# Optimization experiments

Hardware: AMD Instinct MI355X
Metric: run time of the kernel (lower is better)

The kernel has to match this reference:

```python
import jax, jax.numpy as jnp
import numpy as np

N = 32768      # tokens
E = 2048       # embedding_dim
V = 256        # vq_dim
K = 256        # codebook size (levels=[256] -> single level, log2 K = 8)
HID = 1024     # condition MLP hidden dim
LOG2K = 8      # log2_num_embeddings
N_MID = 4      # condition_layer - 2 middle blocks
BN_EPS = 1e-5


def _normalize(x):
    return x / (jnp.linalg.norm(x, axis=-1, keepdims=True) + 1e-6)


def _bn(x, g, b):
    # BatchNorm1d, training-mode batch statistics over the codebook rows
    m = x.mean(0)
    v = x.var(0)
    return g * (x - m) * jax.lax.rsqrt(v + BN_EPS) + b


def _codebook(w0, b0, g0, be0, wm, bm, gm, bem, wL, bL):
    # get_bvectors(8, 256): binary expansion of 0..255, width 8 (no pad needed)
    ints = jnp.arange(K)
    bits = ((ints[:, None] >> jnp.arange(LOG2K - 1, -1, -1)[None, :]) & 1).astype(jnp.float32)
    x = jax.nn.relu(_bn(bits @ w0 + b0, g0, be0))
    for i in range(N_MID):
        x = jax.nn.relu(_bn(x @ wm[i] + bm[i], gm[i], bem[i]))
    return x @ wL + bL  # [K, V]


def setup_inputs() -> dict:
    key = jax.random.key(0)
    ks = jax.random.split(key, 8)
    def lin(k, fan_in, shape):
        return (jax.random.normal(k, shape, jnp.float32) / np.sqrt(fan_in)).astype(jnp.float32)
    return {
        "h_in": jax.random.normal(ks[0], (N, E), jnp.float32),
        "temp": jnp.array([0.3], jnp.float32),
        "proj_w": lin(ks[1], E, (E, V)), "proj_b": jnp.zeros((V,), jnp.float32),
        "pinv_w": lin(ks[2], V, (V, E)), "pinv_b": jnp.zeros((E,), jnp.float32),
        "w0": lin(ks[3], LOG2K, (LOG2K, HID)), "b0": jnp.zeros((HID,), jnp.float32),
        "g0": jnp.ones((HID,), jnp.float32), "be0": jnp.zeros((HID,), jnp.float32),
        "wm": lin(ks[4], HID, (N_MID, HID, HID)), "bm": jnp.zeros((N_MID, HID), jnp.float32),
        "gm": jnp.ones((N_MID, HID), jnp.float32), "bem": jnp.zeros((N_MID, HID), jnp.float32),
        "wL": lin(ks[5], HID, (HID, V)), "bL": jnp.zeros((V,), jnp.float32),
    }


def reference(h_in, temp, proj_w, proj_b, pinv_w, pinv_b,
              w0, b0, g0, be0, wm, bm, gm, bem, wL, bL):
    # forward(h_in, mode='eval', temperature=1, level=256); levels=[256] -> idx_all=1
    h = _normalize(h_in @ proj_w + proj_b)                          # proj + sphere normalize, [N, V]
    embed = _normalize(_codebook(w0, b0, g0, be0, wm, bm, gm, bem, wL, bL))  # [K, V]

    # attention(): distance logits with temperature-scaled detached term
    sim = h @ embed.T                                               # [N, K]
    alpha = 1.0 / temp ** 2
    distances = -2.0 * (alpha - 1.0) * jax.lax.stop_gradient(sim) - 2.0 * sim
    A = jax.nn.softmax(-distances, axis=1)                          # [N, K]

    k_code, k_p = jax.random.split(jax.random.key(42))
    code = jax.random.categorical(k_code, -distances, axis=-1)      # multinomial(A, 1), [N]
    onehot = jax.nn.one_hot(code, K, dtype=A.dtype)
    c = onehot * (1.0 - A) + (1.0 - onehot) * (-A)
    A2 = A + jax.lax.stop_gradient(c)                               # fwd value == onehot
    h_vq = h + A2 @ embed - jax.lax.stop_gradient(h)                # straight-through quantize
    vq_loss = jnp.linalg.norm(h_vq - h, axis=-1).mean()             # idx_all == 1

    # select = (0 < p) & (p < 1) since idx=0, idx_all=1
    p = jax.random.uniform(k_p, (h.shape[0],))
    select = (0.0 < p) & (p < 1.0)
    quantized = h_vq * select[:, None].astype(h_vq.dtype)
    probs = A * select[:, None].astype(A.dtype)
    vq_code = code * select.astype(code.dtype)

    quantized_inv = quantized @ pinv_w + pinv_b                     # [N, E]
    return quantized_inv, vq_code, quantized, probs, vq_loss
```

## Files before the change

### kernel.cpp

```cpp
#include <hip/hip_runtime.h>
#include <hip/hip_bf16.h>
#include <stdint.h>
#include <stddef.h>

#ifndef PARTITIONABLE
#define PARTITIONABLE 1
#endif

typedef __attribute__((ext_vector_type(8))) short short8;
typedef __attribute__((ext_vector_type(4))) short short4v;
typedef __attribute__((ext_vector_type(4))) float f32x4;

__host__ __device__ __forceinline__ uint32_t rotl32(uint32_t x, int d){ return (x<<d)|(x>>(32-d)); }

__host__ __device__ __forceinline__ void tf4(uint32_t&x0, uint32_t&x1, int r0,int r1,int r2,int r3){
  x0+=x1; x1=rotl32(x1,r0); x1^=x0;
  x0+=x1; x1=rotl32(x1,r1); x1^=x0;
  x0+=x1; x1=rotl32(x1,r2); x1^=x0;
  x0+=x1; x1=rotl32(x1,r3); x1^=x0;
}
__host__ __device__ __forceinline__ void threefry2x32(uint32_t k0,uint32_t k1,uint32_t x0,uint32_t x1,
                                                      uint32_t&y0,uint32_t&y1){
  uint32_t ks2 = k0^k1^0x1BD11BDAu;
  x0+=k0; x1+=k1;
  tf4(x0,x1,13,15,26,6);  x0+=k1;  x1+=ks2+1u;
  tf4(x0,x1,17,29,16,24); x0+=ks2; x1+=k0+2u;
  tf4(x0,x1,13,15,26,6);  x0+=k0;  x1+=k1+3u;
  tf4(x0,x1,17,29,16,24); x0+=k1;  x1+=ks2+4u;
  tf4(x0,x1,13,15,26,6);  x0+=ks2; x1+=k0+5u;
  y0=x0; y1=x1;
}

__device__ __forceinline__ uint32_t random_bits32(uint32_t k0,uint32_t k1,uint32_t idx, uint32_t half){
#if PARTITIONABLE
  uint32_t y0,y1; threefry2x32(k0,k1, 0u, idx, y0,y1);
  (void)half;
  return y0 ^ y1;
#else
  uint32_t y0,y1;
  if (idx < half) { threefry2x32(k0,k1, idx, idx+half, y0,y1); return y0; }
  else            { threefry2x32(k0,k1, idx-half, idx, y0,y1); return y1; }
#endif
}

__device__ __forceinline__ unsigned short bf16_rne(float x){
  unsigned u = __float_as_uint(x);
  unsigned r = (u + 0x7FFFu + ((u>>16)&1u)) >> 16;
  return (unsigned short)r;
}
__device__ __forceinline__ float bf16_tof(unsigned short h){
  return __uint_as_float(((unsigned)h)<<16);
}
__device__ __forceinline__ void split8(const float* src, short8& hi, short8& lo){
  #pragma unroll
  for (int e=0;e<8;e++){
    unsigned short h = bf16_rne(src[e]);
    hi[e] = (short)h;
    lo[e] = (short)bf16_rne(src[e] - bf16_tof(h));
  }
}
__device__ __forceinline__ void split4(const float* src, short4v& hi, short4v& lo){
  #pragma unroll
  for (int e=0;e<4;e++){
    unsigned short h = bf16_rne(src[e]);
    hi[e] = (short)h;
    lo[e] = (short)bf16_rne(src[e] - bf16_tof(h));
  }
}

__device__ __forceinline__ void gll16(const void* g, void* l){
  __builtin_amdgcn_global_load_lds(
      (const __attribute__((address_space(1))) unsigned int*)g,
      (__attribute__((address_space(3))) unsigned int*)l, 16, 0, 0);
}

__device__ __forceinline__ void mk1_gemm(const float* __restrict__ A, int lda,
                                         const unsigned short* __restrict__ packB,
                                         int K, char* smem, f32x4 (&acc)[2][4]){
  const int tid=threadIdx.x, lane=tid&63, wv=tid>>6;
  const int wr=wv>>2, wc=wv&3;
  const int arow=tid>>3, aseg=tid&7, swA=(arow>>1)&3;
  unsigned short* Ahi=(unsigned short*)smem;
  unsigned short* Alo=(unsigned short*)(smem+4096);
  unsigned short* Bhi=(unsigned short*)(smem+8192);
  unsigned short* Blo=(unsigned short*)(smem+24576);
  const int NT=K/32;
  const int sA = arow*32 + ((aseg>>1)^swA)*8 + (aseg&1)*4;
  const int seg = wv*2;

  float4 av = *(const float4*)(A + (size_t)arow*lda + aseg*4);
  for(int t=0;t<NT;t++){
    __syncthreads();
    {
      float af[4]={av.x,av.y,av.z,av.w}; short4v vh,vl; split4(af,vh,vl);
      *(short4v*)&Ahi[sA]=vh; *(short4v*)&Alo[sA]=vl;
      const unsigned short* src = packB + (size_t)t*16384;
      #pragma unroll
      for(int q=0;q<2;q++){
        gll16(src + (seg+q)*512 + lane*8,        (char*)Bhi + (seg+q)*1024);
        gll16(src + 8192 + (seg+q)*512 + lane*8, (char*)Blo + (seg+q)*1024);
      }
      if (t+1<NT) av = *(const float4*)(A + (size_t)arow*lda + (t+1)*32 + aseg*4);
    }
    __syncthreads();
    short8 ah[2],al[2],bh[4],bl[4];
    const int kg=lane>>4;
    #pragma unroll
    for(int i=0;i<2;i++){
      const int r = wr*32 + i*16 + (lane&15);
      const int offA = r*32 + ((kg ^ ((r>>1)&3))*8);
      ah[i]=*(const short8*)&Ahi[offA]; al[i]=*(const short8*)&Alo[offA];
    }
    #pragma unroll
    for(int j=0;j<4;j++){
      const int c = wc*64 + j*16 + (lane&15);
      const int offB = c*32 + ((kg ^ ((c>>1)&3))*8);
      bh[j]=*(const short8*)&Bhi[offB]; bl[j]=*(const short8*)&Blo[offB];
    }
    #pragma unroll
    for(int i=0;i<2;i++)
      #pragma unroll
      for(int j=0;j<4;j++){
        acc[i][j]=__builtin_amdgcn_mfma_f32_16x16x32_bf16(ah[i],bh[j],acc[i][j],0,0,0);
        acc[i][j]=__builtin_amdgcn_mfma_f32_16x16x32_bf16(ah[i],bl[j],acc[i][j],0,0,0);
        acc[i][j]=__builtin_amdgcn_mfma_f32_16x16x32_bf16(al[i],bh[j],acc[i][j],0,0,0);
      }
  }
}

__device__ __forceinline__ void bn_block_t(float (&acc)[4], int col0,
                                           const float* __restrict__ gma,
                                           const float* __restrict__ bta,
                                           float* __restrict__ Yt,
                                           float* Zs, float* red, float* mcol, float* vcol){
  const int r = threadIdx.x;
  #pragma unroll
  for (int j=0;j<4;j++) Zs[r*5+j] = acc[j];
  __syncthreads();
  if (r < 16){
    const int rl = r & 3, j = r >> 2;
    float s = 0.f;
    for (int rr=rl; rr<256; rr+=4) s += Zs[rr*5+j];
    red[rl*4+j] = s;
  }
  __syncthreads();
  if (r < 4)
    mcol[r] = (red[0*4+r]+red[1*4+r]+red[2*4+r]+red[3*4+r]) * (1.0f/256.0f);
  __syncthreads();
  if (r < 16){
    const int rl = r & 3, j = r >> 2;
    const float m = mcol[j];
    float s2 = 0.f;
    for (int rr=rl; rr<256; rr+=4){ float d = Zs[rr*5+j]-m; s2 += d*d; }
    red[rl*4+j] = s2;
  }
  __syncthreads();
  if (r < 4)
    vcol[r] = (red[0*4+r]+red[1*4+r]+red[2*4+r]+red[3*4+r]) * (1.0f/256.0f);
  __syncthreads();
  #pragma unroll
  for (int j=0;j<4;j++){
    const int c = col0 + j;
    const float scale = gma[c] * rsqrtf(vcol[j] + 1e-5f);
    const float sh = bta[c];
    const float v = (acc[j]-mcol[j])*scale + sh;
    Yt[(size_t)c*256 + r] = v > 0.f ? v : 0.f;
  }
}

__global__ __launch_bounds__(256) void prep_kernel(
    const float* __restrict__ proj_w, unsigned short* __restrict__ packW,
    const float* __restrict__ w0, const float* __restrict__ b0,
    const float* __restrict__ g0, const float* __restrict__ be0,
    float* __restrict__ XtA){
  __shared__ float Zs[256*5];
  __shared__ float red[16], mcol[4], vcol[4];
  const int b = blockIdx.x, tid = threadIdx.x;
  {
    const int t = b>>2, s = b&3, c = tid;
    const int g = s ^ ((c>>1)&3);
    const float* p = proj_w + (size_t)(t*32 + g*8)*256 + c;
    float bf[8];
    #pragma unroll
    for(int e=0;e<8;e++) bf[e]=p[(size_t)e*256];
    short8 h,l; split8(bf,h,l);
    unsigned short* dst = packW + (size_t)t*16384 + c*32 + s*8;
    *(short8*)dst = h;
    *(short8*)(dst+8192) = l;
  }
  {
    const int col0 = b*4;
    float acc[4];
    #pragma unroll
    for (int j=0;j<4;j++) acc[j] = b0[col0+j];
    #pragma unroll
    for (int jj=0;jj<8;jj++){
      if ((tid >> (7-jj)) & 1){
        #pragma unroll
        for (int j=0;j<4;j++) acc[j] += w0[jj*1024 + col0 + j];
      }
    }
    bn_block_t(acc, col0, g0, be0, XtA, Zs, red, mcol, vcol);
  }
}

__global__ __launch_bounds__(256) void mlp_layer2_kernel(
    const float* __restrict__ Xt, const float* __restrict__ W,
    const float* __restrict__ bias,
    const float* __restrict__ gma, const float* __restrict__ bta,
    float* __restrict__ Yt){
  __shared__ float Ws[1024*2];
  __shared__ float Zs[256*3];
  __shared__ float red[8], mcol[2], vcol[2];
  const int r = threadIdx.x;
  const int col0 = blockIdx.x*2;
  #pragma unroll
  for (int q=0;q<4;q++){
    const int k = q*256 + r;
    const float2 wv = *(const float2*)&W[(size_t)k*1024 + col0];
    *(float2*)&Ws[k*2] = wv;
  }
  __syncthreads();
  float acc0=0.f, acc1=0.f;
  #pragma unroll 32
  for (int k=0;k<1024;k++){
    const float a = Xt[(size_t)k*256 + r];
    acc0 += a*Ws[k*2];
    acc1 += a*Ws[k*2+1];
  }
  acc0 += bias[col0]; acc1 += bias[col0+1];
  Zs[r*3+0]=acc0; Zs[r*3+1]=acc1;
  __syncthreads();
  if (r < 8){
    const int rl = r & 3, j = r >> 2;
    float s=0.f;
    for (int rr=rl; rr<256; rr+=4) s += Zs[rr*3+j];
    red[rl*2+j] = s;
  }
  __syncthreads();
  if (r < 2) mcol[r] = (red[0*2+r]+red[1*2+r]+red[2*2+r]+red[3*2+r])*(1.0f/256.0f);
  __syncthreads();
  if (r < 8){
    const int rl = r & 3, j = r >> 2;
    const float m = mcol[j];
    float s2=0.f;
    for (int rr=rl; rr<256; rr+=4){ float d = Zs[rr*3+j]-m; s2 += d*d; }
    red[rl*2+j] = s2;
  }
  __syncthreads();
  if (r < 2) vcol[r] = (red[0*2+r]+red[1*2+r]+red[2*2+r]+red[3*2+r])*(1.0f/256.0f);
  __syncthreads();
  {
    const float s0 = gma[col0] * rsqrtf(vcol[0] + 1e-5f);
    const float v0 = (acc0-mcol[0])*s0 + bta[col0];
    Yt[(size_t)col0*256 + r] = v0 > 0.f ? v0 : 0.f;
    const float s1 = gma[col0+1] * rsqrtf(vcol[1] + 1e-5f);
    const float v1 = (acc1-mcol[1])*s1 + bta[col0+1];
    Yt[(size_t)(col0+1)*256 + r] = v1 > 0.f ? v1 : 0.f;
  }
}

__global__ __launch_bounds__(256) void mlp_tail_kernel(
    const float* __restrict__ Xt,
    const float* __restrict__ wL, const float* __restrict__ bL,
    const float* __restrict__ pinv_w, const float* __restrict__ pinv_b,
    float* __restrict__ embed, unsigned short* __restrict__ packE,
    float* __restrict__ Epp){
  __shared__ float xrow[1024];
  __shared__ float erow[256];
  __shared__ float wsum[4];
  const int n = blockIdx.x, t = threadIdx.x;
  #pragma unroll
  for (int q=0;q<4;q++) xrow[q*256+t] = Xt[(size_t)(q*256+t)*256 + n];
  __syncthreads();
  float acc = 0.f;
  #pragma unroll 16
  for (int k=0;k<1024;k++) acc += xrow[k] * wL[(size_t)k*256 + t];
  acc += bL[t];
  const int lane = t & 63, wv = t >> 6;
  float v = acc*acc;
  #pragma unroll
  for (int o=32;o;o>>=1) v += __shfl_xor(v,o);
  if (lane==0) wsum[wv]=v;
  __syncthreads();
  const float total = wsum[0]+wsum[1]+wsum[2]+wsum[3];
  const float inv = 1.0f/(sqrtf(total)+1e-6f);
  const float y = acc*inv;
  embed[(size_t)n*256+t] = y;
  erow[t] = y;
  {
    unsigned short h = bf16_rne(y);
    unsigned short l = bf16_rne(y - bf16_tof(h));
    const int tt=t>>5, kk=t&31, g=kk>>3, e=kk&7, s=g^((n>>1)&3);
    unsigned short* d = packE + (size_t)tt*16384 + n*32 + s*8 + e;
    d[0] = h; d[8192] = l;
  }
  __syncthreads();
  float a8[8] = {0.f,0.f,0.f,0.f,0.f,0.f,0.f,0.f};
  #pragma unroll 8
  for (int k=0;k<256;k++){
    const float ev = erow[k];
    const float4 w0v = *(const float4*)&pinv_w[(size_t)k*2048 + t*8];
    const float4 w1v = *(const float4*)&pinv_w[(size_t)k*2048 + t*8 + 4];
    a8[0] += ev*w0v.x; a8[1] += ev*w0v.y; a8[2] += ev*w0v.z; a8[3] += ev*w0v.w;
    a8[4] += ev*w1v.x; a8[5] += ev*w1v.y; a8[6] += ev*w1v.z; a8[7] += ev*w1v.w;
  }
  #pragma unroll
  for (int j=0;j<8;j++) a8[j] += pinv_b[t*8+j];
  float4* dst = (float4*)(Epp + (size_t)n*2048 + t*8);
  dst[0] = (float4){a8[0],a8[1],a8[2],a8[3]};
  dst[1] = (float4){a8[4],a8[5],a8[6],a8[7]};
}

__global__ __launch_bounds__(512) void proj_norm_kernel(
    const float* __restrict__ A, const unsigned short* __restrict__ packW,
    const float* __restrict__ bias, float* __restrict__ Hn, int K){
  __shared__ char smem[40960];
  f32x4 acc[2][4];
  #pragma unroll
  for (int i=0;i<2;i++)
    #pragma unroll
    for (int j=0;j<4;j++) acc[i][j] = (f32x4){0.f,0.f,0.f,0.f};
  const int bm = blockIdx.x * 64;
  mk1_gemm(A + (size_t)bm*K, K, packW, K, smem, acc);
  __syncthreads();

  const int tid = threadIdx.x, lane = tid&63, wv = tid>>6;
  const int wr = wv>>2, wc = wv&3;
  float* ns = (float*)smem;
  #pragma unroll
  for (int j=0;j<4;j++){
    const int c = wc*64 + j*16 + (lane&15);
    const float bb = bias[c];
    #pragma unroll
    for (int i=0;i<2;i++)
      #pragma unroll
      for (int reg=0;reg<4;reg++) acc[i][j][reg] += bb;
  }
  #pragma unroll
  for (int i=0;i<2;i++)
    #pragma unroll
    for (int reg=0;reg<4;reg++){
      float p = acc[i][0][reg]*acc[i][0][reg] + acc[i][1][reg]*acc[i][1][reg]
              + acc[i][2][reg]*acc[i][2][reg] + acc[i][3][reg]*acc[i][3][reg];
      #pragma unroll
      for (int o=1;o<16;o<<=1) p += __shfl_xor(p, o);
      if ((lane&15)==0) ns[wc*64 + wr*32 + i*16 + (lane>>4)*4 + reg] = p;
    }
  __syncthreads();
  #pragma unroll
  for (int i=0;i<2;i++){
    const int rl = wr*32 + i*16 + (lane>>4)*4;
    #pragma unroll
    for (int reg=0;reg<4;reg++){
      const int r = rl + reg;
      const float tot = ns[0*64+r]+ns[1*64+r]+ns[2*64+r]+ns[3*64+r];
      const float inv = 1.0f/(sqrtf(tot)+1e-6f);
      const size_t grow = (size_t)(bm + r);
      #pragma unroll
      for (int j=0;j<4;j++){
        const int c = wc*64 + j*16 + (lane&15);
        Hn[grow*256 + c] = acc[i][j][reg]*inv;
      }
    }
  }
}

__global__ __launch_bounds__(512) void sim_sample_kernel(
    const float* __restrict__ Hn, const unsigned short* __restrict__ packE,
    const float* __restrict__ embed, const float* __restrict__ temp,
    float* __restrict__ probs, float* __restrict__ codef,
    float* __restrict__ quant, float* __restrict__ norms,
    const float* __restrict__ Epp, const float* __restrict__ pinv_b,
    float* __restrict__ q_inv,
    uint32_t kc0, uint32_t kc1, uint32_t kp0, uint32_t kp1){
  __shared__ char smem[40960];
  f32x4 acc[2][4];
  #pragma unroll
  for (int i=0;i<2;i++)
    #pragma unroll
    for (int j=0;j<4;j++) acc[i][j] = (f32x4){0.f,0.f,0.f,0.f};
  const int bm = blockIdx.x * 64;
  mk1_gemm(Hn + (size_t)bm*256, 256, packE, 256, smem, acc);
  __syncthreads();

  float* redf = (float*)smem;
  int*   redi = (int*)(smem+1024);
  float* smax = (float*)(smem+2048);
  float* ssum = (float*)(smem+2304);
  float* ssel = (float*)(smem+2560);
  int*  scode = (int*)(smem+2816);

  const int tid = threadIdx.x, lane = tid&63, wv = tid>>6;
  const int wr = wv>>2, wc = wv&3;
  const float tv = temp[0];
  const float alpha = 1.0f/(tv*tv);
  #pragma unroll
  for (int i=0;i<2;i++)
    #pragma unroll
    for (int j=0;j<4;j++)
      #pragma unroll
      for (int reg=0;reg<4;reg++){
        const float s = acc[i][j][reg];
        const float dist = -2.0f*(alpha-1.0f)*s - 2.0f*s;
        acc[i][j][reg] = -dist;
      }
  #pragma unroll
  for (int i=0;i<2;i++)
    #pragma unroll
    for (int reg=0;reg<4;reg++){
      float m = fmaxf(fmaxf(acc[i][0][reg], acc[i][1][reg]),
                      fmaxf(acc[i][2][reg], acc[i][3][reg]));
      #pragma unroll
      for (int o=1;o<16;o<<=1) m = fmaxf(m, __shfl_xor(m, o));
      if ((lane&15)==0) redf[wc*64 + wr*32 + i*16 + (lane>>4)*4 + reg] = m;
    }
  __syncthreads();
  if (tid < 64)
    smax[tid] = fmaxf(fmaxf(redf[0*64+tid], redf[1*64+tid]), fmaxf(redf[2*64+tid], redf[3*64+tid]));
  __syncthreads();
  #pragma unroll
  for (int i=0;i<2;i++)
    #pragma unroll
    for (int reg=0;reg<4;reg++){
      const int r = wr*32 + i*16 + (lane>>4)*4 + reg;
      const float m = smax[r];
      float p = expf(acc[i][0][reg]-m) + expf(acc[i][1][reg]-m)
              + expf(acc[i][2][reg]-m) + expf(acc[i][3][reg]-m);
      #pragma unroll
      for (int o=1;o<16;o<<=1) p += __shfl_xor(p, o);
      if ((lane&15)==0) redf[wc*64 + r] = p;
    }
  __syncthreads();
  if (tid < 64){
    ssum[tid] = redf[0*64+tid]+redf[1*64+tid]+redf[2*64+tid]+redf[3*64+tid];
    const uint32_t pb = random_bits32(kp0,kp1,(uint32_t)(bm+tid), 16384u);
    const float pf = __uint_as_float((pb>>9) | 0x3f800000u) - 1.0f;
    ssel[tid] = (pf > 0.0f) ? 1.0f : 0.0f;
  }
  __syncthreads();
  #pragma unroll
  for (int i=0;i<2;i++)
    #pragma unroll
    for (int reg=0;reg<4;reg++){
      const int r = wr*32 + i*16 + (lane>>4)*4 + reg;
      const uint32_t grow = (uint32_t)(bm + r);
      float zb = -1e38f; int ib = 0x7fffffff;
      #pragma unroll
      for (int j=0;j<4;j++){
        const int c = wc*64 + j*16 + (lane&15);
        const uint32_t bits = random_bits32(kc0,kc1, grow*256u + (uint32_t)c, 4194304u);
        const float f = __uint_as_float((bits>>9) | 0x3f800000u) - 1.0f;
        const float TINY = 1.17549435082228751e-38f;
        const float u = fmaxf(TINY, f + TINY);
        const float g = -logf(-logf(u));
        const float z = acc[i][j][reg] + g;
        if (z > zb || (z == zb && c < ib)){ zb = z; ib = c; }
      }
      #pragma unroll
      for (int o=1;o<16;o<<=1){
        const float zo = __shfl_xor(zb, o); const int io = __shfl_xor(ib, o);
        if (zo > zb || (zo == zb && io < ib)){ zb = zo; ib = io; }
      }
      if ((lane&15)==0){ redf[wc*64 + r] = zb; redi[wc*64 + r] = ib; }
    }
  __syncthreads();
  if (tid < 64){
    float zb = redf[0*64+tid]; int ib = redi[0*64+tid];
    #pragma unroll
    for (int w=1; w<4; w++)
      if (redf[w*64+tid] > zb || (redf[w*64+tid] == zb && redi[w*64+tid] < ib)){
        zb = redf[w*64+tid]; ib = redi[w*64+tid];
      }
    scode[tid] = ib;
  }
  __syncthreads();
  #pragma unroll
  for (int i=0;i<2;i++)
    #pragma unroll
    for (int reg=0;reg<4;reg++){
      const int r = wr*32 + i*16 + (lane>>4)*4 + reg;
      const size_t grow = (size_t)(bm + r);
      const float m = smax[r], sum = ssum[r], sel = ssel[r];
      const int code = scode[r];
      float p2 = 0.f;
      #pragma unroll
      for (int j=0;j<4;j++){
        const int c = wc*64 + j*16 + (lane&15);
        const float e = expf(acc[i][j][reg] - m);
        probs[grow*256 + c] = (e/sum) * sel;
        const float ev = embed[(size_t)code*256 + c];
        quant[grow*256 + c] = ev * sel;
        const float d = ev - Hn[grow*256 + c];
        p2 += d*d;
      }
      #pragma unroll
      for (int o=1;o<16;o<<=1) p2 += __shfl_xor(p2, o);
      if ((lane&15)==0) redf[wc*64 + r] = p2;
    }
  __syncthreads();
  if (tid < 64){
    norms[bm+tid] = sqrtf(redf[0*64+tid]+redf[1*64+tid]+redf[2*64+tid]+redf[3*64+tid]);
    codef[bm+tid] = (float)scode[tid] * ssel[tid];
  }
  #pragma unroll
  for (int rr=0; rr<8; rr++){
    const int r = wv*8 + rr;
    const int code = scode[r];
    const float sel = ssel[r];
    const float4* s4 = (const float4*)((sel != 0.0f) ? (Epp + (size_t)code*2048) : pinv_b);
    float4* dst = (float4*)(q_inv + (size_t)(bm + r)*2048);
    #pragma unroll
    for (int q=0;q<8;q++) dst[q*64 + lane] = s4[q*64 + lane];
  }
}

__global__ __launch_bounds__(256) void loss_kernel(const float* __restrict__ norms,
                                                   float* __restrict__ outp){
  const int t = threadIdx.x;
  float s = 0.f;
  for (int i=t;i<32768;i+=256) s += norms[i];
  #pragma unroll
  for (int o=32;o;o>>=1) s += __shfl_xor(s,o);
  __shared__ float wred[4];
  if ((t&63)==0) wred[t>>6]=s;
  __syncthreads();
  if (t==0) outp[0] = (wred[0]+wred[1]+wred[2]+wred[3]) * (1.0f/32768.0f);
}

extern "C" void kernel_launch(void* const* d_in, const int* in_sizes, int n_in,
                              void* d_out, int out_size, void* d_ws, size_t ws_size,
                              hipStream_t stream){
  const float* h_in  = (const float*)d_in[0];
  const float* temp  = (const float*)d_in[1];
  const float* proj_w= (const float*)d_in[2];
  const float* proj_b= (const float*)d_in[3];
  const float* pinv_w= (const float*)d_in[4];
  const float* pinv_b= (const float*)d_in[5];
  const float* w0 = (const float*)d_in[6];
  const float* b0 = (const float*)d_in[7];
  const float* g0 = (const float*)d_in[8];
  const float* be0= (const float*)d_in[9];
  const float* wm = (const float*)d_in[10];
  const float* bm = (const float*)d_in[11];
  const float* gm = (const float*)d_in[12];
  const float* bem= (const float*)d_in[13];
  const float* wL = (const float*)d_in[14];
  const float* bL = (const float*)d_in[15];

  float* out = (float*)d_out;
  float* q_inv  = out;
  float* o_code = out + 67108864;
  float* o_quant= out + 67141632;
  float* o_probs= out + 75530240;
  float* o_loss = out + 83918848;

  float* ws = (float*)d_ws;
  float* Hn     = ws + 0;
  float* XtA    = ws + 8388608;
  float* XtB    = ws + 8650752;
  float* embed  = ws + 8912896;
  float* norms  = ws + 8978432;
  float* Epp    = ws + 9076736;
  unsigned short* packW = (unsigned short*)(ws + 9601024);
  unsigned short* packE = (unsigned short*)(ws + 10125312);

  uint32_t kc0,kc1,kp0,kp1;
#if PARTITIONABLE
  threefry2x32(0u,42u, 0u,0u, kc0,kc1);
  threefry2x32(0u,42u, 0u,1u, kp0,kp1);
#else
  { uint32_t a0,b0w,a1,b1w;
    threefry2x32(0u,42u, 0u,2u, a0,b0w);
    threefry2x32(0u,42u, 1u,3u, a1,b1w);
    kc0=a0; kc1=a1; kp0=b0w; kp1=b1w; }
#endif

  prep_kernel<<<256,256,0,stream>>>(proj_w, packW, w0, b0, g0, be0, XtA);

  proj_norm_kernel<<<512,512,0,stream>>>(h_in, packW, proj_b, Hn, 2048);

  mlp_layer2_kernel<<<512,256,0,stream>>>(XtA, wm + 0*1048576, bm + 0*1024, gm + 0*1024, bem + 0*1024, XtB);
  mlp_layer2_kernel<<<512,256,0,stream>>>(XtB, wm + 1*1048576, bm + 1*1024, gm + 1*1024, bem + 1*1024, XtA);
  mlp_layer2_kernel<<<512,256,0,stream>>>(XtA, wm + 2*1048576, bm + 2*1024, gm + 2*1024, bem + 2*1024, XtB);
  mlp_layer2_kernel<<<512,256,0,stream>>>(XtB, wm + 3*1048576, bm + 3*1024, gm + 3*1024, bem + 3*1024, XtA);
  mlp_tail_kernel<<<256,256,0,stream>>>(XtA, wL, bL, pinv_w, pinv_b, embed, packE, Epp);

  sim_sample_kernel<<<512,512,0,stream>>>(Hn, packE, embed, temp,
                                          o_probs, o_code, o_quant, norms,
                                          Epp, pinv_b, q_inv,
                                          kc0,kc1,kp0,kp1);
  loss_kernel<<<1,256,0,stream>>>(norms, o_loss);
}
```

Baseline: 517.8 us.

## Co-schedule projection GEMM tiles with codebook MLP layers in shared launches

Splits the 512-block projection+normalize kernel into four quarters and fuses each quarter with one codebook MLP middle layer into a single heterogeneous launch. Blocks 0-127 run projection tiles while the remaining 256 blocks each compute two MLP column pairs with 512 threads. The goal is to fill the GPU during the small, latency-bound MLP layers with independent projection work and to cut kernel launches. The cost is that the larger shared-memory and register footprint of the GEMM path now applies to the MLP blocks, and the two block types may not balance.

```diff
diff --git a/kernel.cpp b/kernel.cpp
--- a/kernel.cpp
+++ b/kernel.cpp
@@ -128,6 +128,126 @@
   }
 }
 
+__device__ __forceinline__ void proj_tile(const float* __restrict__ A,
+    const unsigned short* __restrict__ packW, const float* __restrict__ bias,
+    float* __restrict__ Hn, int K, int bm, char* smem){
+  f32x4 acc[2][4];
+  #pragma unroll
+  for (int i=0;i<2;i++)
+    #pragma unroll
+    for (int j=0;j<4;j++) acc[i][j] = (f32x4){0.f,0.f,0.f,0.f};
+  mk1_gemm(A + (size_t)bm*K, K, packW, K, smem, acc);
+  __syncthreads();
+
+  const int tid = threadIdx.x, lane = tid&63, wv = tid>>6;
+  const int wr = wv>>2, wc = wv&3;
+  float* ns = (float*)smem;
+  #pragma unroll
+  for (int j=0;j<4;j++){
+    const int c = wc*64 + j*16 + (lane&15);
+    const float bb = bias[c];
+    #pragma unroll
+    for (int i=0;i<2;i++)
+      #pragma unroll
+      for (int reg=0;reg<4;reg++) acc[i][j][reg] += bb;
+  }
+  #pragma unroll
+  for (int i=0;i<2;i++)
+    #pragma unroll
+    for (int reg=0;reg<4;reg++){
+      float p = acc[i][0][reg]*acc[i][0][reg] + acc[i][1][reg]*acc[i][1][reg]
+              + acc[i][2][reg]*acc[i][2][reg] + acc[i][3][reg]*acc[i][3][reg];
+      #pragma unroll
+      for (int o=1;o<16;o<<=1) p += __shfl_xor(p, o);
+      if ((lane&15)==0) ns[wc*64 + wr*32 + i*16 + (lane>>4)*4 + reg] = p;
+    }
+  __syncthreads();
+  #pragma unroll
+  for (int i=0;i<2;i++){
+    const int rl = wr*32 + i*16 + (lane>>4)*4;
+    #pragma unroll
+    for (int reg=0;reg<4;reg++){
+      const int r = rl + reg;
+      const float tot = ns[0*64+r]+ns[1*64+r]+ns[2*64+r]+ns[3*64+r];
+      const float inv = 1.0f/(sqrtf(tot)+1e-6f);
+      const size_t grow = (size_t)(bm + r);
+      #pragma unroll
+      for (int j=0;j<4;j++){
+        const int c = wc*64 + j*16 + (lane&15);
+        Hn[grow*256 + c] = acc[i][j][reg]*inv;
+      }
+    }
+  }
+}
+
+__global__ __launch_bounds__(512) void proj_mid_kernel(
+    const float* __restrict__ A, const unsigned short* __restrict__ packW,
+    const float* __restrict__ proj_b, float* __restrict__ Hn, int K, int qi,
+    const float* __restrict__ Xt, const float* __restrict__ W,
+    const float* __restrict__ bias,
+    const float* __restrict__ gma, const float* __restrict__ bta,
+    float* __restrict__ Yt){
+  __shared__ char smem[40960];
+  const int b = blockIdx.x;
+  if (b < 128){
+    proj_tile(A, packW, proj_b, Hn, K, (qi*128 + b)*64, smem);
+    return;
+  }
+  const int mb = b - 128;
+  const int tid = threadIdx.x;
+  const int r = tid & 255, g = tid >> 8;
+  const int col0 = mb*2 + g*512;
+  float* Ws   = (float*)smem + g*2048;
+  float* Zs   = (float*)(smem + 16384) + g*768;
+  float* red  = (float*)(smem + 22528) + g*8;
+  float* mcol = (float*)(smem + 22592) + g*2;
+  float* vcol = (float*)(smem + 22608) + g*2;
+  #pragma unroll
+  for (int q=0;q<4;q++){
+    const int k = q*256 + r;
+    const float2 wv = *(const float2*)&W[(size_t)k*1024 + col0];
+    *(float2*)&Ws[k*2] = wv;
+  }
+  __syncthreads();
+  float acc0=0.f, acc1=0.f;
+  #pragma unroll 32
+  for (int k=0;k<1024;k++){
+    const float a = Xt[(size_t)k*256 + r];
+    acc0 += a*Ws[k*2];
+    acc1 += a*Ws[k*2+1];
+  }
+  acc0 += bias[col0]; acc1 += bias[col0+1];
+  Zs[r*3+0]=acc0; Zs[r*3+1]=acc1;
+  __syncthreads();
+  if (r < 8){
+    const int rl = r & 3, j = r >> 2;
+    float s=0.f;
+    for (int rr=rl; rr<256; rr+=4) s += Zs[rr*3+j];
+    red[rl*2+j] = s;
+  }
+  __syncthreads();
+  if (r < 2) mcol[r] = (red[0*2+r]+red[1*2+r]+red[2*2+r]+red[3*2+r])*(1.0f/256.0f);
+  __syncthreads();
+  if (r < 8){
+    const int rl = r & 3, j = r >> 2;
+    const float m = mcol[j];
+    float s2=0.f;
+    for (int rr=rl; rr<256; rr+=4){ float d = Zs[rr*3+j]-m; s2 += d*d; }
+    red[rl*2+j] = s2;
+  }
+  __syncthreads();
+  if (r < 2) vcol[r] = (red[0*2+r]+red[1*2+r]+red[2*2+r]+red[3*2+r])*(1.0f/256.0f);
+  __syncthreads();
+  {
+    const float s0 = gma[col0] * rsqrtf(vcol[0] + 1e-5f);
+    const float v0 = (acc0-mcol[0])*s0 + bta[col0];
+    Yt[(size_t)col0*256 + r] = v0 > 0.f ? v0 : 0.f;
+    const float s1 = gma[col0+1] * rsqrtf(vcol[1] + 1e-5f);
+    const float v1 = (acc1-mcol[1])*s1 + bta[col0+1];
+    Yt[(size_t)(col0+1)*256 + r] = v1 > 0.f ? v1 : 0.f;
+  }
+}
+
 __device__ __forceinline__ void bn_block_t(float (&acc)[4], int col0,
                                            const float* __restrict__ gma,
                                            const float* __restrict__ bta,
@@ -204,62 +324,6 @@
   }
 }
 
-__global__ __launch_bounds__(256) void mlp_layer2_kernel(
-    const float* __restrict__ Xt, const float* __restrict__ W,
-    const float* __restrict__ bias,
-    const float* __restrict__ gma, const float* __restrict__ bta,
-    float* __restrict__ Yt){
-  __shared__ float Ws[1024*2];
-  __shared__ float Zs[256*3];
-  __shared__ float red[8], mcol[2], vcol[2];
-  const int r = threadIdx.x;
-  const int col0 = blockIdx.x*2;
-  #pragma unroll
-  for (int q=0;q<4;q++){
-    const int k = q*256 + r;
-    const float2 wv = *(const float2*)&W[(size_t)k*1024 + col0];
-    *(float2*)&Ws[k*2] = wv;
-  }
-  __syncthreads();
-  float acc0=0.f, acc1=0.f;
-  #pragma unroll 32
-  for (int k=0;k<1024;k++){
-    const float a = Xt[(size_t)k*256 + r];
-    acc0 += a*Ws[k*2];
-    acc1 += a*Ws[k*2+1];
-  }
-  acc0 += bias[col0]; acc1 += bias[col0+1];
-  Zs[r*3+0]=acc0; Zs[r*3+1]=acc1;
-  __syncthreads();
-  if (r < 8){
-    const int rl = r & 3, j = r >> 2;
-    float s=0.f;
-    for (int rr=rl; rr<256; rr+=4) s += Zs[rr*3+j];
-    red[rl*2+j] = s;
-  }
-  __syncthreads();
-  if (r < 2) mcol[r] = (red[0*2+r]+red[1*2+r]+red[2*2+r]+red[3*2+r])*(1.0f/256.0f);
-  __syncthreads();
-  if (r < 8){
-    const int rl = r & 3, j = r >> 2;
-    const float m = mcol[j];
-    float s2=0.f;
-    for (int rr=rl; rr<256; rr+=4){ float d = Zs[rr*3+j]-m; s2 += d*d; }
-    red[rl*2+j] = s2;
-  }
-  __syncthreads();
-  if (r < 2) vcol[r] = (red[0*2+r]+red[1*2+r]+red[2*2+r]+red[3*2+r])*(1.0f/256.0f);
-  __syncthreads();
-  {
-    const float s0 = gma[col0] * rsqrtf(vcol[0] + 1e-5f);
-    const float v0 = (acc0-mcol[0])*s0 + bta[col0];
-    Yt[(size_t)col0*256 + r] = v0 > 0.f ? v0 : 0.f;
-    const float s1 = gma[col0+1] * rsqrtf(vcol[1] + 1e-5f);
-    const float v1 = (acc1-mcol[1])*s1 + bta[col0+1];
-    Yt[(size_t)(col0+1)*256 + r] = v1 > 0.f ? v1 : 0.f;
-  }
-}
-
 __global__ __launch_bounds__(256) void mlp_tail_kernel(
     const float* __restrict__ Xt,
     const float* __restrict__ wL, const float* __restrict__ bL,
@@ -310,60 +374,6 @@
   float4* dst = (float4*)(Epp + (size_t)n*2048 + t*8);
   dst[0] = (float4){a8[0],a8[1],a8[2],a8[3]};
   dst[1] = (float4){a8[4],a8[5],a8[6],a8[7]};
-}
-
-__global__ __launch_bounds__(512) void proj_norm_kernel(
-    const float* __restrict__ A, const unsigned short* __restrict__ packW,
-    const float* __restrict__ bias, float* __restrict__ Hn, int K){
-  __shared__ char smem[40960];
-  f32x4 acc[2][4];
-  #pragma unroll
-  for (int i=0;i<2;i++)
-    #pragma unroll
-    for (int j=0;j<4;j++) acc[i][j] = (f32x4){0.f,0.f,0.f,0.f};
-  const int bm = blockIdx.x * 64;
-  mk1_gemm(A + (size_t)bm*K, K, packW, K, smem, acc);
-  __syncthreads();
-
-  const int tid = threadIdx.x, lane = tid&63, wv = tid>>6;
-  const int wr = wv>>2, wc = wv&3;
-  float* ns = (float*)smem;
-  #pragma unroll
-  for (int j=0;j<4;j++){
-    const int c = wc*64 + j*16 + (lane&15);
-    const float bb = bias[c];
-    #pragma unroll
-    for (int i=0;i<2;i++)
-      #pragma unroll
-      for (int reg=0;reg<4;reg++) acc[i][j][reg] += bb;
-  }
-  #pragma unroll
-  for (int i=0;i<2;i++)
-    #pragma unroll
-    for (int reg=0;reg<4;reg++){
-      float p = acc[i][0][reg]*acc[i][0][reg] + acc[i][1][reg]*acc[i][1][reg]
-              + acc[i][2][reg]*acc[i][2][reg] + acc[i][3][reg]*acc[i][3][reg];
-      #pragma unroll
-      for (int o=1;o<16;o<<=1) p += __shfl_xor(p, o);
-      if ((lane&15)==0) ns[wc*64 + wr*32 + i*16 + (lane>>4)*4 + reg] = p;
-    }
-  __syncthreads();
-  #pragma unroll
-  for (int i=0;i<2;i++){
-    const int rl = wr*32 + i*16 + (lane>>4)*4;
-    #pragma unroll
-    for (int reg=0;reg<4;reg++){
-      const int r = rl + reg;
-      const float tot = ns[0*64+r]+ns[1*64+r]+ns[2*64+r]+ns[3*64+r];
-      const float inv = 1.0f/(sqrtf(tot)+1e-6f);
-      const size_t grow = (size_t)(bm + r);
-      #pragma unroll
-      for (int j=0;j<4;j++){
-        const int c = wc*64 + j*16 + (lane&15);
-        Hn[grow*256 + c] = acc[i][j][reg]*inv;
-      }
-    }
-  }
 }
 
 __global__ __launch_bounds__(512) void sim_sample_kernel(
@@ -578,12 +588,15 @@
 
   prep_kernel<<<256,256,0,stream>>>(proj_w, packW, w0, b0, g0, be0, XtA);
 
-  proj_norm_kernel<<<512,512,0,stream>>>(h_in, packW, proj_b, Hn, 2048);
-
-  mlp_layer2_kernel<<<512,256,0,stream>>>(XtA, wm + 0*1048576, bm + 0*1024, gm + 0*1024, bem + 0*1024, XtB);
-  mlp_layer2_kernel<<<512,256,0,stream>>>(XtB, wm + 1*1048576, bm + 1*1024, gm + 1*1024, bem + 1*1024, XtA);
-  mlp_layer2_kernel<<<512,256,0,stream>>>(XtA, wm + 2*1048576, bm + 2*1024, gm + 2*1024, bem + 2*1024, XtB);
-  mlp_layer2_kernel<<<512,256,0,stream>>>(XtB, wm + 3*1048576, bm + 3*1024, gm + 3*1024, bem + 3*1024, XtA);
+  proj_mid_kernel<<<384,512,0,stream>>>(h_in, packW, proj_b, Hn, 2048, 0,
+                                        XtA, wm + 0*1048576, bm + 0*1024, gm + 0*1024, bem + 0*1024, XtB);
+  proj_mid_kernel<<<384,512,0,stream>>>(h_in, packW, proj_b, Hn, 2048, 1,
+                                        XtB, wm + 1*1048576, bm + 1*1024, gm + 1*1024, bem + 1*1024, XtA);
+  proj_mid_kernel<<<384,512,0,stream>>>(h_in, packW, proj_b, Hn, 2048, 2,
+                                        XtA, wm + 2*1048576, bm + 2*1024, gm + 2*1024, bem + 2*1024, XtB);
+  proj_mid_kernel<<<384,512,0,stream>>>(h_in, packW, proj_b, Hn, 2048, 3,
+                                        XtB, wm + 3*1048576, bm + 3*1024, gm + 3*1024, bem + 3*1024, XtA);
+
   mlp_tail_kernel<<<256,256,0,stream>>>(XtA, wL, bL, pinv_w, pinv_b, embed, packE, Epp);
 
   sim_sample_kernel<<<512,512,0,stream>>>(Hn, packE, embed, temp,
```

Measured after the change: 631.7 us. 22.0% more time.
